# Performance work log

Measured on AMD Instinct MI355X. Metric: run time of the kernel, lower is better.

The kernel has to match this reference:

```python
import jax, jax.numpy as jnp
import numpy as np

B, N, T, D = 16, 30, 50, 4
K, H, M, NH = 4, 128, 128, 128
E = N * (N - 1)  # 870


def setup_inputs() -> dict:
    key = jax.random.key(0)
    ks = jax.random.split(key, 12)
    # one-hot receiver / sender matrices for fully connected graph (no self loops)
    pairs = np.array([(i, j) for i in range(N) for j in range(N) if i != j])
    eye = np.eye(N, dtype=np.float32)
    rel_rec = jnp.asarray(eye[pairs[:, 0]])   # [E, N]
    rel_send = jnp.asarray(eye[pairs[:, 1]])  # [E, N]
    s = 0.1
    return {
        "inputs": jax.random.normal(ks[0], (B, N, T, D), jnp.float32),
        "rel_type": jax.random.uniform(ks[1], (B, E, K), jnp.float32),
        "rel_rec": rel_rec,
        "rel_send": rel_send,
        "W1": jax.random.normal(ks[2], (K, 2 * D, H), jnp.float32) * s,
        "b1": jax.random.normal(ks[3], (K, H), jnp.float32) * s,
        "W2": jax.random.normal(ks[4], (K, H, M), jnp.float32) * s,
        "b2": jax.random.normal(ks[5], (K, M), jnp.float32) * s,
        "oW1": jax.random.normal(ks[6], (D + M, NH), jnp.float32) * s,
        "ob1": jax.random.normal(ks[7], (NH,), jnp.float32) * s,
        "oW2": jax.random.normal(ks[8], (NH, NH), jnp.float32) * s,
        "ob2": jax.random.normal(ks[9], (NH,), jnp.float32) * s,
        "oW3": jax.random.normal(ks[10], (NH, D), jnp.float32) * s,
        "ob3": jax.random.normal(ks[11], (D,), jnp.float32) * s,
        "pred_steps": 1,
    }


def _single_step(x, rt, rel_rec, rel_send, W1, b1, W2, b2, oW1, ob1, oW2, ob2, oW3, ob3):
    # x: [B, Ts, N, D], rt: [B, Ts, E, K]
    recv = jnp.einsum('en,btnd->bted', rel_rec, x)
    send = jnp.einsum('en,btnd->bted', rel_send, x)
    pre_msg = jnp.concatenate([recv, send], axis=-1)           # [B,Ts,E,2D]
    all_msgs = jnp.zeros(pre_msg.shape[:-1] + (M,), x.dtype)
    for k in range(K):  # small fixed set of structurally distinct MLPs
        msg = jax.nn.relu(pre_msg @ W1[k] + b1[k])
        msg = jax.nn.relu(msg @ W2[k] + b2[k])
        all_msgs = all_msgs + msg * rt[..., k:k + 1]
    agg = jnp.einsum('btef,en->btnf', all_msgs, rel_rec)       # scatter-sum to receivers
    aug = jnp.concatenate([x, agg], axis=-1)                    # [B,Ts,N,D+M]
    h = jax.nn.relu(aug @ oW1 + ob1)
    h = jax.nn.relu(h @ oW2 + ob2)
    return x + (h @ oW3 + ob3)


def reference(inputs, rel_type, rel_rec, rel_send, W1, b1, W2, b2,
              oW1, ob1, oW2, ob2, oW3, ob3, pred_steps):
    x = jnp.transpose(inputs, (0, 2, 1, 3))                    # [B,T,N,D]
    Tt = x.shape[1]
    rt = jnp.broadcast_to(rel_type[:, None], (rel_type.shape[0], Tt) + rel_type.shape[1:])
    last_pred = x[:, 0::pred_steps]
    curr_rt = rt[:, 0::pred_steps]
    preds = []
    for _ in range(pred_steps):
        last_pred = _single_step(last_pred, curr_rt, rel_rec, rel_send,
                                 W1, b1, W2, b2, oW1, ob1, oW2, ob2, oW3, ob3)
        preds.append(last_pred)
    Ts = preds[0].shape[1]
    out = jnp.stack(preds, axis=2).reshape(x.shape[0], Ts * pred_steps, x.shape[2], x.shape[3])
    pred_all = out[:, :Tt - 1]
    return jnp.transpose(pred_all, (0, 2, 1, 3))               # [B,N,T-1,D]
```

## Files before the change

kernel.cpp:

```cpp
#include <hip/hip_runtime.h>

typedef __bf16 bf16_t;
typedef __bf16 bf16x8 __attribute__((ext_vector_type(8)));
typedef __bf16 bf16x4 __attribute__((ext_vector_type(4)));
typedef float  f32x4  __attribute__((ext_vector_type(4)));

#define NB 16
#define NN 30
#define NT 50
#define ND 4
#define NK 4
#define NE 870

#define C_INPUTS   0
#define C_RELTYPE  96000
#define C_B2       152192
#define C_OB1      152704
#define C_OB2      152832
#define C_OW3      152960
#define C_OB3      153472
#define C_W1F      153480
#define C_W2F      169864
#define C_OW1F     235400
#define C_OW2F     255880
#define AGG_BYTE_OFF (1u << 20)

__device__ __forceinline__ bf16x8 bzero8() {
  bf16x8 z;
#pragma unroll
  for (int j = 0; j < 8; ++j) z[j] = (bf16_t)0.0f;
  return z;
}

__device__ __forceinline__ f32x4 make4(float a, float b, float c, float d) {
  f32x4 v; v[0] = a; v[1] = b; v[2] = c; v[3] = d; return v;
}

__device__ __forceinline__ void pack_store4(bf16_t* dst, f32x4 a) {
  bf16x4 v;
  v[0] = (bf16_t)fmaxf(a[0], 0.0f);
  v[1] = (bf16_t)fmaxf(a[1], 0.0f);
  v[2] = (bf16_t)fmaxf(a[2], 0.0f);
  v[3] = (bf16_t)fmaxf(a[3], 0.0f);
  *(bf16x4*)dst = v;
}

__device__ __forceinline__ int detect_isbf16(const void* p) {
  const unsigned short* w = (const unsigned short*)p;
  int c = 0;
#pragma unroll 4
  for (int i = 0; i < 256; i += 2) {
    const int e = (w[i] >> 7) & 0xFF;
    if (e >= 100 && e <= 150) ++c;
  }
  return c >= 96;
}

__device__ __forceinline__ float ldf(const void* src, int idx, int isbf) {
  return isbf ? (float)((const bf16_t*)src)[idx] : ((const float*)src)[idx];
}

__device__ __forceinline__ void conv_arr(const void* src, bf16_t* dst, int n,
                                         int isbf, int gtid, int gsz) {
  if (isbf) {
    const unsigned short* s = (const unsigned short*)src;
    unsigned short* d = (unsigned short*)dst;
    for (int i = gtid; i < n; i += gsz) d[i] = s[i];
  } else {
    const float* s = (const float*)src;
    for (int i = gtid; i < n; i += gsz) dst[i] = (bf16_t)s[i];
  }
}

__global__ void convert_kernel(const void* inputs, const void* rel_type,
                               const void* W1, const void* b1,
                               const void* W2, const void* b2,
                               const void* oW1, const void* ob1,
                               const void* oW2, const void* ob2,
                               const void* oW3, const void* ob3,
                               void* ws)
{
  __shared__ int sflag;
  if (threadIdx.x == 0) sflag = detect_isbf16(inputs);
  __syncthreads();
  const int isbf = sflag;
  if (blockIdx.x == 0 && threadIdx.x == 0) *(int*)ws = isbf;
  bf16_t* cb = (bf16_t*)((char*)ws + 16);
  const int gtid = blockIdx.x * blockDim.x + threadIdx.x;
  const int gsz  = gridDim.x * blockDim.x;

  conv_arr(inputs,   cb + C_INPUTS,  96000, isbf, gtid, gsz);
  conv_arr(rel_type, cb + C_RELTYPE, 55680, isbf, gtid, gsz);
  conv_arr(b2,  cb + C_B2,  512, isbf, gtid, gsz);
  conv_arr(ob1, cb + C_OB1, 128, isbf, gtid, gsz);
  conv_arr(ob2, cb + C_OB2, 128, isbf, gtid, gsz);
  conv_arr(oW3, cb + C_OW3, 512, isbf, gtid, gsz);
  conv_arr(ob3, cb + C_OB3, 4,   isbf, gtid, gsz);

  for (int i = gtid; i < 16384; i += gsz) {
    const int j = i & 7, lm = (i >> 3) & 15, quad = (i >> 7) & 3;
    const int ct = (i >> 9) & 7, k = (i >> 12) & 3;
    float v = 0.0f;
    if (quad == 0)                 v = ldf(W1, k * 1024 + j * 128 + ct * 16 + lm, isbf);
    else if (quad == 1 && j == 0)  v = ldf(b1, k * 128 + ct * 16 + lm, isbf);
    cb[C_W1F + i] = (bf16_t)v;
  }
  for (int i = gtid; i < 65536; i += gsz) {
    const int j = i & 7;
    const int l64 = (i >> 3) & 63;
    const int ct = (i >> 9) & 7, kc = (i >> 12) & 3, k = (i >> 14) & 3;
    const int quad = l64 >> 4, lm = l64 & 15;
    const int kk = kc * 32 + quad * 8 + j;
    cb[C_W2F + i] = (bf16_t)ldf(W2, k * 16384 + kk * 128 + ct * 16 + lm, isbf);
  }
  for (int i = gtid; i < 20480; i += gsz) {
    const int j = i & 7, lm = (i >> 3) & 15, quad = (i >> 7) & 3;
    const int rem = i >> 9;
    const int kc = rem % 5, ct = rem / 5;
    const int kk = kc * 32 + quad * 8 + j;
    float v = 0.0f;
    if (kk < 132) v = ldf(oW1, kk * 128 + ct * 16 + lm, isbf);
    cb[C_OW1F + i] = (bf16_t)v;
  }
  for (int i = gtid; i < 16384; i += gsz) {
    const int j = i & 7, lm = (i >> 3) & 15, quad = (i >> 7) & 3;
    const int kc = (i >> 9) & 3, ct = (i >> 11) & 7;
    const int kk = kc * 32 + quad * 8 + j;
    cb[C_OW2F + i] = (bf16_t)ldf(oW2, kk * 128 + ct * 16 + lm, isbf);
  }
}

struct EdgeSmem {
  union { bf16_t h[8192]; float aggf[2048]; } u;
  bf16_t sfrag[7168];
  bf16_t xl[128];
};

__global__ __launch_bounds__(256)
void edge_kernel(const bf16_t* __restrict__ inputs,
                 const bf16_t* __restrict__ rel_type,
                 const bf16_t* __restrict__ w1f_g,
                 const bf16_t* __restrict__ w2f_g,
                 const bf16_t* __restrict__ b2c,
                 float* __restrict__ aggbuf)
{
  __shared__ EdgeSmem s;
  const int tid  = threadIdx.x;
  const int bid  = blockIdx.x;
  const int nhalf = bid & 1;
  const int bt   = bid >> 1;
  const int b    = bt / NT;
  const int t    = bt - b * NT;
  const int wave = tid >> 6;
  const int lane = tid & 63;
  const int quad = lane >> 4;
  const int lm   = lane & 15;
  const int ctbase = (wave & 1) * 4;
  const int spair  = (wave >> 1) * 2;

  if (tid < 30) {
    *(uint2*)&s.xl[tid * 4] = *(const uint2*)&inputs[((b * NN + tid) * NT + t) * ND];
  }
  for (int i = tid; i < 896; i += 256) *(bf16x8*)&s.sfrag[i * 8] = bzero8();
  __syncthreads();

  const int e0g = b * NE + nhalf * 435;
  f32x4 aggacc[4];
#pragma unroll
  for (int c = 0; c < 4; ++c) aggacc[c] = make4(0.f, 0.f, 0.f, 0.f);

#pragma unroll 1
  for (int k = 0; k < NK; ++k) {
    bf16x8 w1r[4];
    bf16x8 w2r[4][4];
    float  b2s[4];
#pragma unroll
    for (int c = 0; c < 4; ++c) {
      const int ct = ctbase + c;
      w1r[c] = *(const bf16x8*)&w1f_g[(((k * 8 + ct) * 4 + quad) * 16 + lm) * 8];
#pragma unroll
      for (int kc = 0; kc < 4; ++kc)
        w2r[c][kc] = *(const bf16x8*)&w2f_g[((((k * 4 + kc) * 8) + ct) * 64 + quad * 16 + lm) * 8];
      b2s[c] = (float)b2c[k * 128 + ct * 16 + lm];
    }
    for (int i = tid; i < 435; i += 256) {
      const int slot = ((i >> 4) * 64 + ((i >> 2) & 3) * 16 + i / 29) * 4 + (i & 3);
      s.sfrag[slot] = rel_type[(e0g + i) * 4 + k];
    }

#pragma unroll 1
    for (int tt = 0; tt < 7; ++tt) {
#pragma unroll
      for (int si = 0; si < 2; ++si) {
        const int strip = spair + si;
        const int rr = strip * 16 + lm;
        const int e  = tt * 64 + rr;
        bf16x8 pm = bzero8();
        if (quad == 0) {
          if (e < 435) {
            const int recv = nhalf * 15 + e / 29;
            const int j29  = e % 29;
            const int send = j29 + (j29 >= recv);
            union { uint2 u2[2]; bf16x8 v; } c;
            c.u2[0] = *(const uint2*)&s.xl[recv * 4];
            c.u2[1] = *(const uint2*)&s.xl[send * 4];
            pm = c.v;
          }
        } else if (quad == 1) {
          pm[0] = (bf16_t)1.0f;
        }
        const f32x4 z4 = make4(0.0f, 0.0f, 0.0f, 0.0f);
#pragma unroll
        for (int c = 0; c < 4; ++c) {
          const int ct = ctbase + c;
          f32x4 a1 = __builtin_amdgcn_mfma_f32_16x16x32_bf16(w1r[c], pm, z4, 0, 0, 0);
          const int qr = 2 * (ct & 1) + (quad >> 1);
          pack_store4(&s.u.h[((strip * 4 + (ct >> 1)) * 64 + qr * 16 + lm) * 8 + 4 * (quad & 1)], a1);
        }
      }
      __syncthreads();

#pragma unroll
      for (int si = 0; si < 2; ++si) {
        const int strip = spair + si;
        bf16x8 af[4];
#pragma unroll
        for (int kc = 0; kc < 4; ++kc)
          af[kc] = *(const bf16x8*)&s.u.h[((strip * 4 + kc) * 64 + quad * 16 + lm) * 8];
        bf16x8 sa = bzero8();
        {
          const bf16x4 s4 = *(const bf16x4*)&s.sfrag[((tt * 4 + strip) * 64 + lane) * 4];
          sa[0] = s4[0]; sa[1] = s4[1]; sa[2] = s4[2]; sa[3] = s4[3];
        }
#pragma unroll
        for (int c = 0; c < 4; ++c) {
          f32x4 acc = make4(b2s[c], b2s[c], b2s[c], b2s[c]);
#pragma unroll
          for (int kc = 0; kc < 4; ++kc)
            acc = __builtin_amdgcn_mfma_f32_16x16x32_bf16(af[kc], w2r[c][kc], acc, 0, 0, 0);
          bf16x8 mb = bzero8();
          mb[0] = (bf16_t)fmaxf(acc[0], 0.0f);
          mb[1] = (bf16_t)fmaxf(acc[1], 0.0f);
          mb[2] = (bf16_t)fmaxf(acc[2], 0.0f);
          mb[3] = (bf16_t)fmaxf(acc[3], 0.0f);
          aggacc[c] = __builtin_amdgcn_mfma_f32_16x16x32_bf16(sa, mb, aggacc[c], 0, 0, 0);
        }
      }
      __syncthreads();
    }
  }

  for (int i = tid; i < 2048; i += 256) s.u.aggf[i] = 0.0f;
  __syncthreads();
#pragma unroll
  for (int c = 0; c < 4; ++c)
#pragma unroll
    for (int r = 0; r < 4; ++r)
      atomicAdd(&s.u.aggf[(quad * 4 + r) * 128 + (ctbase + c) * 16 + lm], aggacc[c][r]);
  __syncthreads();
  for (int i = tid; i < 15 * 128; i += 256) {
    const int r = i >> 7, col = i & 127;
    aggbuf[(size_t)(bt * NN + nhalf * 15 + r) * 128 + col] = s.u.aggf[r * 128 + col];
  }
}

struct NodeSmem {
  bf16_t h1[64 * 136];
  bf16_t h2[64 * 136];
  bf16_t xres[64 * 4];
  float  b1f[128];
  float  b2f[128];
  float  w3f[128 * 4];
  float  b3f[4];
};

__global__ __launch_bounds__(256)
void node_kernel(const bf16_t* __restrict__ inputs,
                 const bf16_t* __restrict__ ow1f_g, const bf16_t* __restrict__ ob1,
                 const bf16_t* __restrict__ ow2f_g, const bf16_t* __restrict__ ob2,
                 const bf16_t* __restrict__ oW3, const bf16_t* __restrict__ ob3,
                 const int* __restrict__ flagptr,
                 const float* __restrict__ aggbuf,
                 void* __restrict__ outp)
{
  __shared__ NodeSmem s;
  const int tid  = threadIdx.x;
  const int wave = tid >> 6;
  const int lane = tid & 63;
  const int quad = lane >> 4;
  const int lm   = lane & 15;
  const int row  = wave * 16 + lm;
  const int r0   = blockIdx.x * 64;
  const int isbf = *flagptr;

  if (tid < 64) {
    const int r  = r0 + tid;
    const int n  = r % NN;
    const int bt = r / NN;
    const int t  = bt % NT;
    const int b  = bt / NT;
    *(uint2*)&s.xres[tid * 4] = *(const uint2*)&inputs[((b * NN + n) * NT + t) * ND];
  }
  if (tid < 128) s.b1f[tid] = (float)ob1[tid];
  else           s.b2f[tid - 128] = (float)ob2[tid - 128];
  if (tid < 4) s.b3f[tid] = (float)ob3[tid];
  for (int i = tid; i < 512; i += 256) s.w3f[i] = (float)oW3[i];
  __syncthreads();

  bf16x8 bfa[5];
  {
    const float* aggrow = aggbuf + (size_t)(r0 + row) * 128;
    float tmp[8];
    if (quad == 0) {
#pragma unroll
      for (int j = 0; j < 4; ++j) tmp[j] = (float)s.xres[row * 4 + j];
      const float4 a = *(const float4*)(aggrow);
      tmp[4] = a.x; tmp[5] = a.y; tmp[6] = a.z; tmp[7] = a.w;
    } else {
      const int c0 = quad * 8 - 4;
      const float4 a = *(const float4*)(aggrow + c0);
      const float4 d = *(const float4*)(aggrow + c0 + 4);
      tmp[0] = a.x; tmp[1] = a.y; tmp[2] = a.z; tmp[3] = a.w;
      tmp[4] = d.x; tmp[5] = d.y; tmp[6] = d.z; tmp[7] = d.w;
    }
#pragma unroll
    for (int j = 0; j < 8; ++j) bfa[0][j] = (bf16_t)tmp[j];
#pragma unroll
    for (int kc = 1; kc < 4; ++kc) {
      const int c0 = kc * 32 + quad * 8 - 4;
      const float4 a = *(const float4*)(aggrow + c0);
      const float4 d = *(const float4*)(aggrow + c0 + 4);
      tmp[0] = a.x; tmp[1] = a.y; tmp[2] = a.z; tmp[3] = a.w;
      tmp[4] = d.x; tmp[5] = d.y; tmp[6] = d.z; tmp[7] = d.w;
#pragma unroll
      for (int j = 0; j < 8; ++j) bfa[kc][j] = (bf16_t)tmp[j];
    }
    if (quad == 0) {
      const float4 a = *(const float4*)(aggrow + 124);
      tmp[0] = a.x; tmp[1] = a.y; tmp[2] = a.z; tmp[3] = a.w;
      tmp[4] = 0.f; tmp[5] = 0.f; tmp[6] = 0.f; tmp[7] = 0.f;
#pragma unroll
      for (int j = 0; j < 8; ++j) bfa[4][j] = (bf16_t)tmp[j];
    } else bfa[4] = bzero8();
  }

#pragma unroll
  for (int ct = 0; ct < 8; ++ct) {
    const int nb = ct * 16 + quad * 4;
    f32x4 acc = make4(s.b1f[nb], s.b1f[nb + 1], s.b1f[nb + 2], s.b1f[nb + 3]);
#pragma unroll
    for (int kc = 0; kc < 5; ++kc) {
      const bf16x8 w = *(const bf16x8*)&ow1f_g[(((ct * 5 + kc) * 4 + quad) * 16 + lm) * 8];
      acc = __builtin_amdgcn_mfma_f32_16x16x32_bf16(w, bfa[kc], acc, 0, 0, 0);
    }
    pack_store4(&s.h1[row * 136 + ct * 16 + quad * 4], acc);
  }

  bf16x8 af[4];
#pragma unroll
  for (int kc = 0; kc < 4; ++kc)
    af[kc] = *(const bf16x8*)&s.h1[row * 136 + kc * 32 + quad * 8];

#pragma unroll
  for (int ct = 0; ct < 8; ++ct) {
    const int mb = ct * 16 + quad * 4;
    f32x4 acc = make4(s.b2f[mb], s.b2f[mb + 1], s.b2f[mb + 2], s.b2f[mb + 3]);
#pragma unroll
    for (int kc = 0; kc < 4; ++kc) {
      const bf16x8 w = *(const bf16x8*)&ow2f_g[(((ct * 4 + kc) * 4 + quad) * 16 + lm) * 8];
      acc = __builtin_amdgcn_mfma_f32_16x16x32_bf16(w, af[kc], acc, 0, 0, 0);
    }
    pack_store4(&s.h2[row * 136 + ct * 16 + quad * 4], acc);
  }

  {
    const int rloc = tid >> 2;
    const int d    = tid & 3;
    float a3 = s.b3f[d];
#pragma unroll
    for (int g = 0; g < 16; ++g) {
      const bf16x8 hv = *(const bf16x8*)&s.h2[rloc * 136 + g * 8];
#pragma unroll
      for (int j = 0; j < 8; ++j)
        a3 += (float)hv[j] * s.w3f[(g * 8 + j) * 4 + d];
    }
    a3 += (float)s.xres[rloc * 4 + d];
    const int r  = r0 + rloc;
    const int n  = r % NN;
    const int bt = r / NN;
    const int t  = bt % NT;
    const int b  = bt / NT;
    if (t < NT - 1) {
      const int oidx = ((b * NN + n) * (NT - 1) + t) * ND + d;
      if (isbf) ((bf16_t*)outp)[oidx] = (bf16_t)a3;
      else      ((float*)outp)[oidx]  = a3;
    }
  }
}

extern "C" void kernel_launch(void* const* d_in, const int* in_sizes, int n_in,
                              void* d_out, int out_size, void* d_ws, size_t ws_size,
                              hipStream_t stream) {
  char* ws = (char*)d_ws;
  bf16_t* cb = (bf16_t*)(ws + 16);
  float* aggbuf = (float*)(ws + AGG_BYTE_OFF);

  convert_kernel<<<dim3(256), dim3(256), 0, stream>>>(
      d_in[0], d_in[1], d_in[4], d_in[5], d_in[6], d_in[7],
      d_in[8], d_in[9], d_in[10], d_in[11], d_in[12], d_in[13], d_ws);

  edge_kernel<<<dim3(NB * NT * 2), dim3(256), 0, stream>>>(
      cb + C_INPUTS, cb + C_RELTYPE, cb + C_W1F, cb + C_W2F,
      cb + C_B2, aggbuf);

  node_kernel<<<dim3((NB * NT * NN) / 64), dim3(256), 0, stream>>>(
      cb + C_INPUTS, cb + C_OW1F, cb + C_OB1, cb + C_OW2F, cb + C_OB2,
      cb + C_OW3, cb + C_OB3, (const int*)d_ws, aggbuf, d_out);
}
```

Measured before the change: 345.3 us.

## Keep edge-MLP hidden activations in registers via lane permutes instead of LDS

The edge kernel now gives each wave a whole 16-edge strip across all 8 column tiles. The layer-1 outputs are rearranged into layer-2 A-fragments in registers with permlane swaps, with a shuffle fallback, so the LDS staging buffer and both per-tile __syncthreads go away. rel_type is also transposed to a k-major layout during conversion so the per-k loads are contiguous. The cost is twice as many weight registers per thread (8x4 W2 fragments) and a launch-bounds hint of 2 blocks per SM, which raises register pressure and spill risk.

```diff
diff --git a/kernel.cpp b/kernel.cpp
--- a/kernel.cpp
+++ b/kernel.cpp
@@ -25,6 +25,9 @@
 #define C_OW2F     255880
 #define AGG_BYTE_OFF (1u << 20)
 
+union U4 { unsigned w[4]; bf16x8 v; };
+union U2 { unsigned w[2]; bf16x4 v; };
+
 __device__ __forceinline__ bf16x8 bzero8() {
   bf16x8 z;
 #pragma unroll
@@ -43,6 +46,27 @@
   v[2] = (bf16_t)fmaxf(a[2], 0.0f);
   v[3] = (bf16_t)fmaxf(a[3], 0.0f);
   *(bf16x4*)dst = v;
+}
+
+__device__ __forceinline__ void qswap(unsigned x, unsigned y,
+                                      unsigned& zlo, unsigned& zhi) {
+#if __has_builtin(__builtin_amdgcn_permlane32_swap) && __has_builtin(__builtin_amdgcn_permlane16_swap)
+  auto t = __builtin_amdgcn_permlane32_swap(x, y, false, false);
+  auto z = __builtin_amdgcn_permlane16_swap(t[0], t[1], false, false);
+  zlo = z[0]; zhi = z[1];
+#else
+  const int lane = threadIdx.x & 63;
+  const int quad = lane >> 4;
+  const int lm   = lane & 15;
+  const int s0 = (((2 * quad) & 3) << 4) + lm;
+  const int s1 = (((2 * quad + 1) & 3) << 4) + lm;
+  const unsigned a0 = (unsigned)__shfl((int)x, s0, 64);
+  const unsigned b0 = (unsigned)__shfl((int)y, s0, 64);
+  const unsigned a1 = (unsigned)__shfl((int)x, s1, 64);
+  const unsigned b1 = (unsigned)__shfl((int)y, s1, 64);
+  zlo = (quad < 2) ? a0 : b0;
+  zhi = (quad < 2) ? a1 : b1;
+#endif
 }
 
 __device__ __forceinline__ int detect_isbf16(const void* p) {
@@ -90,7 +114,13 @@
   const int gsz  = gridDim.x * blockDim.x;
 
   conv_arr(inputs,   cb + C_INPUTS,  96000, isbf, gtid, gsz);
-  conv_arr(rel_type, cb + C_RELTYPE, 55680, isbf, gtid, gsz);
+  for (int i = gtid; i < 55680; i += gsz) {
+    const int bq  = i / (NK * NE);
+    const int rem = i - bq * (NK * NE);
+    const int k   = rem / NE;
+    const int e   = rem - k * NE;
+    cb[C_RELTYPE + i] = (bf16_t)ldf(rel_type, (bq * NE + e) * NK + k, isbf);
+  }
   conv_arr(b2,  cb + C_B2,  512, isbf, gtid, gsz);
   conv_arr(ob1, cb + C_OB1, 128, isbf, gtid, gsz);
   conv_arr(ob2, cb + C_OB2, 128, isbf, gtid, gsz);
@@ -131,132 +161,143 @@
 }
 
 struct EdgeSmem {
-  union { bf16_t h[8192]; float aggf[2048]; } u;
-  bf16_t sfrag[7168];
+  union { bf16_t sfrag[7168]; float aggf[2048]; } u;
   bf16_t xl[128];
 };
 
-__global__ __launch_bounds__(256)
+__global__ __launch_bounds__(256, 2)
 void edge_kernel(const bf16_t* __restrict__ inputs,
-                 const bf16_t* __restrict__ rel_type,
+                 const bf16_t* __restrict__ rtT,
                  const bf16_t* __restrict__ w1f_g,
                  const bf16_t* __restrict__ w2f_g,
                  const bf16_t* __restrict__ b2c,
                  float* __restrict__ aggbuf)
 {
   __shared__ EdgeSmem s;
-  const int tid  = threadIdx.x;
-  const int bid  = blockIdx.x;
+  const int tid   = threadIdx.x;
+  const int bid   = blockIdx.x;
   const int nhalf = bid & 1;
-  const int bt   = bid >> 1;
-  const int b    = bt / NT;
-  const int t    = bt - b * NT;
-  const int wave = tid >> 6;
-  const int lane = tid & 63;
-  const int quad = lane >> 4;
-  const int lm   = lane & 15;
-  const int ctbase = (wave & 1) * 4;
-  const int spair  = (wave >> 1) * 2;
-
-  if (tid < 30) {
+  const int bt    = bid >> 1;
+  const int b     = bt / NT;
+  const int t     = bt - b * NT;
+  const int wave  = tid >> 6;
+  const int lane  = tid & 63;
+  const int quad  = lane >> 4;
+  const int lm    = lane & 15;
+
+  if (tid < 30)
     *(uint2*)&s.xl[tid * 4] = *(const uint2*)&inputs[((b * NN + tid) * NT + t) * ND];
-  }
-  for (int i = tid; i < 896; i += 256) *(bf16x8*)&s.sfrag[i * 8] = bzero8();
-  __syncthreads();
-
-  const int e0g = b * NE + nhalf * 435;
-  f32x4 aggacc[4];
-#pragma unroll
-  for (int c = 0; c < 4; ++c) aggacc[c] = make4(0.f, 0.f, 0.f, 0.f);
+  if (tid < 8) s.xl[120 + tid] = (bf16_t)0.0f;
+
+  {
+    bf16x4 z; z[0] = z[1] = z[2] = z[3] = (bf16_t)0.0f;
+#pragma unroll
+    for (int s7 = 0; s7 < 7; ++s7)
+      *(bf16x4*)&s.u.sfrag[((s7 * 4 + wave) * 64 + lane) * 4] = z;
+  }
+  __syncthreads();
+
+  f32x4 aggacc[8];
+#pragma unroll
+  for (int ct = 0; ct < 8; ++ct) aggacc[ct] = make4(0.f, 0.f, 0.f, 0.f);
 
 #pragma unroll 1
   for (int k = 0; k < NK; ++k) {
-    bf16x8 w1r[4];
-    bf16x8 w2r[4][4];
-    float  b2s[4];
-#pragma unroll
-    for (int c = 0; c < 4; ++c) {
-      const int ct = ctbase + c;
-      w1r[c] = *(const bf16x8*)&w1f_g[(((k * 8 + ct) * 4 + quad) * 16 + lm) * 8];
+    bf16x8 w1r[8];
+    bf16x8 w2r[8][4];
+    float  b2s[8];
+#pragma unroll
+    for (int ct = 0; ct < 8; ++ct) {
+      w1r[ct] = *(const bf16x8*)&w1f_g[(((k * 8 + ct) * 4 + quad) * 16 + lm) * 8];
 #pragma unroll
       for (int kc = 0; kc < 4; ++kc)
-        w2r[c][kc] = *(const bf16x8*)&w2f_g[((((k * 4 + kc) * 8) + ct) * 64 + quad * 16 + lm) * 8];
-      b2s[c] = (float)b2c[k * 128 + ct * 16 + lm];
-    }
-    for (int i = tid; i < 435; i += 256) {
-      const int slot = ((i >> 4) * 64 + ((i >> 2) & 3) * 16 + i / 29) * 4 + (i & 3);
-      s.sfrag[slot] = rel_type[(e0g + i) * 4 + k];
+        w2r[ct][kc] = *(const bf16x8*)&w2f_g[((((k * 4 + kc) * 8) + ct) * 64 + quad * 16 + lm) * 8];
+      b2s[ct] = (float)b2c[k * 128 + ct * 16 + lm];
+    }
+
+    {
+      const bf16_t* rtk = rtT + (size_t)(b * NK + k) * NE + nhalf * 435;
+#pragma unroll
+      for (int it = 0; it < 2; ++it) {
+        const int idx = it * 64 + lane;
+        const int s7  = idx >> 4;
+        if (s7 < 7) {
+          const int g = s7 * 4 + wave;
+          const int i = g * 16 + (idx & 15);
+          if (i < 435) {
+            const int n    = i / 29;
+            const int slot = (g * 64 + ((i >> 2) & 3) * 16 + n) * 4 + (i & 3);
+            s.u.sfrag[slot] = rtk[i];
+          }
+        }
+      }
     }
 
 #pragma unroll 1
     for (int tt = 0; tt < 7; ++tt) {
-#pragma unroll
-      for (int si = 0; si < 2; ++si) {
-        const int strip = spair + si;
-        const int rr = strip * 16 + lm;
-        const int e  = tt * 64 + rr;
-        bf16x8 pm = bzero8();
-        if (quad == 0) {
-          if (e < 435) {
-            const int recv = nhalf * 15 + e / 29;
-            const int j29  = e % 29;
-            const int send = j29 + (j29 >= recv);
-            union { uint2 u2[2]; bf16x8 v; } c;
-            c.u2[0] = *(const uint2*)&s.xl[recv * 4];
-            c.u2[1] = *(const uint2*)&s.xl[send * 4];
-            pm = c.v;
-          }
-        } else if (quad == 1) {
-          pm[0] = (bf16_t)1.0f;
-        }
-        const f32x4 z4 = make4(0.0f, 0.0f, 0.0f, 0.0f);
-#pragma unroll
-        for (int c = 0; c < 4; ++c) {
-          const int ct = ctbase + c;
-          f32x4 a1 = __builtin_amdgcn_mfma_f32_16x16x32_bf16(w1r[c], pm, z4, 0, 0, 0);
-          const int qr = 2 * (ct & 1) + (quad >> 1);
-          pack_store4(&s.u.h[((strip * 4 + (ct >> 1)) * 64 + qr * 16 + lm) * 8 + 4 * (quad & 1)], a1);
-        }
+      const int g = tt * 4 + wave;
+
+      bf16x8 pm = bzero8();
+      if (quad == 0) {
+        const int e    = g * 16 + lm;
+        const int d29  = e / 29;
+        const int recv = nhalf * 15 + d29;
+        const int j29  = e - d29 * 29;
+        const int send = j29 + (j29 >= recv);
+        union { uint2 u2[2]; bf16x8 v; } c;
+        c.u2[0] = *(const uint2*)&s.xl[recv * 4];
+        c.u2[1] = *(const uint2*)&s.xl[send * 4];
+        pm = c.v;
+      } else if (quad == 1) {
+        pm[0] = (bf16_t)1.0f;
       }
-      __syncthreads();
-
-#pragma unroll
-      for (int si = 0; si < 2; ++si) {
-        const int strip = spair + si;
-        bf16x8 af[4];
+
+      U4 af[4];
+      const f32x4 z4 = make4(0.f, 0.f, 0.f, 0.f);
+#pragma unroll
+      for (int kc = 0; kc < 4; ++kc) {
+        f32x4 aA = __builtin_amdgcn_mfma_f32_16x16x32_bf16(w1r[2 * kc],     pm, z4, 0, 0, 0);
+        f32x4 aB = __builtin_amdgcn_mfma_f32_16x16x32_bf16(w1r[2 * kc + 1], pm, z4, 0, 0, 0);
+        U2 pA, pB;
+        pA.v[0] = (bf16_t)fmaxf(aA[0], 0.f); pA.v[1] = (bf16_t)fmaxf(aA[1], 0.f);
+        pA.v[2] = (bf16_t)fmaxf(aA[2], 0.f); pA.v[3] = (bf16_t)fmaxf(aA[3], 0.f);
+        pB.v[0] = (bf16_t)fmaxf(aB[0], 0.f); pB.v[1] = (bf16_t)fmaxf(aB[1], 0.f);
+        pB.v[2] = (bf16_t)fmaxf(aB[2], 0.f); pB.v[3] = (bf16_t)fmaxf(aB[3], 0.f);
+        qswap(pA.w[0], pB.w[0], af[kc].w[0], af[kc].w[2]);
+        qswap(pA.w[1], pB.w[1], af[kc].w[1], af[kc].w[3]);
+      }
+
+      U4 sa;
+      {
+        U2 s4;
+        s4.v = *(const bf16x4*)&s.u.sfrag[(g * 64 + lane) * 4];
+        sa.w[0] = s4.w[0]; sa.w[1] = s4.w[1]; sa.w[2] = 0u; sa.w[3] = 0u;
+      }
+
+#pragma unroll
+      for (int ct = 0; ct < 8; ++ct) {
+        f32x4 acc = make4(b2s[ct], b2s[ct], b2s[ct], b2s[ct]);
 #pragma unroll
         for (int kc = 0; kc < 4; ++kc)
-          af[kc] = *(const bf16x8*)&s.u.h[((strip * 4 + kc) * 64 + quad * 16 + lm) * 8];
-        bf16x8 sa = bzero8();
-        {
-          const bf16x4 s4 = *(const bf16x4*)&s.sfrag[((tt * 4 + strip) * 64 + lane) * 4];
-          sa[0] = s4[0]; sa[1] = s4[1]; sa[2] = s4[2]; sa[3] = s4[3];
-        }
-#pragma unroll
-        for (int c = 0; c < 4; ++c) {
-          f32x4 acc = make4(b2s[c], b2s[c], b2s[c], b2s[c]);
-#pragma unroll
-          for (int kc = 0; kc < 4; ++kc)
-            acc = __builtin_amdgcn_mfma_f32_16x16x32_bf16(af[kc], w2r[c][kc], acc, 0, 0, 0);
-          bf16x8 mb = bzero8();
-          mb[0] = (bf16_t)fmaxf(acc[0], 0.0f);
-          mb[1] = (bf16_t)fmaxf(acc[1], 0.0f);
-          mb[2] = (bf16_t)fmaxf(acc[2], 0.0f);
-          mb[3] = (bf16_t)fmaxf(acc[3], 0.0f);
-          aggacc[c] = __builtin_amdgcn_mfma_f32_16x16x32_bf16(sa, mb, aggacc[c], 0, 0, 0);
-        }
+          acc = __builtin_amdgcn_mfma_f32_16x16x32_bf16(af[kc].v, w2r[ct][kc], acc, 0, 0, 0);
+        U4 mb;
+        U2 pk;
+        pk.v[0] = (bf16_t)fmaxf(acc[0], 0.f); pk.v[1] = (bf16_t)fmaxf(acc[1], 0.f);
+        pk.v[2] = (bf16_t)fmaxf(acc[2], 0.f); pk.v[3] = (bf16_t)fmaxf(acc[3], 0.f);
+        mb.w[0] = pk.w[0]; mb.w[1] = pk.w[1]; mb.w[2] = 0u; mb.w[3] = 0u;
+        aggacc[ct] = __builtin_amdgcn_mfma_f32_16x16x32_bf16(sa.v, mb.v, aggacc[ct], 0, 0, 0);
       }
-      __syncthreads();
-    }
-  }
-
+    }
+  }
+
+  __syncthreads();
   for (int i = tid; i < 2048; i += 256) s.u.aggf[i] = 0.0f;
   __syncthreads();
 #pragma unroll
-  for (int c = 0; c < 4; ++c)
+  for (int ct = 0; ct < 8; ++ct)
 #pragma unroll
     for (int r = 0; r < 4; ++r)
-      atomicAdd(&s.u.aggf[(quad * 4 + r) * 128 + (ctbase + c) * 16 + lm], aggacc[c][r]);
+      atomicAdd(&s.u.aggf[(quad * 4 + r) * 128 + ct * 16 + lm], aggacc[ct][r]);
   __syncthreads();
   for (int i = tid; i < 15 * 128; i += 256) {
     const int r = i >> 7, col = i & 127;
```

Result: faster. 335.9 us (-2.7%).
